# Optimization experiments

Measured on AMD Instinct MI355X. Metric: run time of the kernel, lower is better.

The kernel has to match this reference:

```python
import jax, jax.numpy as jnp
import numpy as np

N_EMBD = 768

def setup_inputs() -> dict:
    key = jax.random.key(0)
    k1, k2, k3, k4 = jax.random.split(key, 4)
    B, T, head_size = 16, 1024, 128
    x = jax.random.normal(k1, (B, T, N_EMBD), dtype=jnp.float32)
    # nn.Linear(in, out, bias=False): weight stored as (out, in); we store transposed (in, out)
    s = 1.0 / np.sqrt(N_EMBD)
    Wk = jax.random.uniform(k2, (N_EMBD, head_size), jnp.float32, -s, s)
    Wq = jax.random.uniform(k3, (N_EMBD, head_size), jnp.float32, -s, s)
    Wv = jax.random.uniform(k4, (N_EMBD, head_size), jnp.float32, -s, s)
    return {"x": x, "Wk": Wk, "Wq": Wq, "Wv": Wv}

def reference(x, Wk, Wq, Wv):
    B, T, C = x.shape  # C == n_embd == 768
    k = jnp.einsum('btc,ch->bth', x, Wk)
    q = jnp.einsum('btc,ch->bth', x, Wq)
    v = jnp.einsum('btc,ch->bth', x, Wv)
    # NOTE: original scales by C**-0.5 with C = n_embd (768), not head_size.
    wei = jnp.einsum('bth,bsh->bts', q, k) * (C ** -0.5)  # (B, T, T)
    causal = jnp.tril(jnp.ones((T, T), dtype=bool))
    wei = jnp.where(causal, wei, -jnp.inf)
    wei = jax.nn.softmax(wei, axis=-1)
    # dropout p=0.0 -> identity
    return jnp.einsum('bts,bsh->bth', wei, v)
```

## Files before the change

kernel.cpp:

```cpp
#include <hip/hip_runtime.h>
#include <hip/hip_bf16.h>
#include <math.h>

#define NTOK   16384
#define NEMBD  768
#define HDIM   128

typedef __attribute__((ext_vector_type(8)))  short short8;
typedef __attribute__((ext_vector_type(16))) float floatx16;

#define MFMA32(a,b,c) __builtin_amdgcn_mfma_f32_32x32x16_bf16(a,b,c,0,0,0)

__device__ __forceinline__ unsigned short f2bf(float f) {
    unsigned u = __float_as_uint(f);
    u += 0x7fff + ((u >> 16) & 1);
    return (unsigned short)(u >> 16);
}
__device__ __forceinline__ unsigned pack2(float a, float b) {
    __hip_bfloat162 h2 = __float22bfloat162_rn(make_float2(a, b));
    union { __hip_bfloat162 h; unsigned u; } c; c.h = h2;
    return c.u;
}
__device__ __forceinline__ unsigned pack2_trunc(float a, float b) {
    return __builtin_amdgcn_perm(__float_as_uint(b), __float_as_uint(a),
                                 0x07060302u);
}
__device__ __forceinline__ void gl_lds16(const void* gptr, void* lptr) {
    __builtin_amdgcn_global_load_lds(
        (const __attribute__((address_space(1))) unsigned int*)gptr,
        (__attribute__((address_space(3))) unsigned int*)lptr, 16, 0, 0);
}

__global__ __launch_bounds__(256) void prep_w(
    const float* __restrict__ Wk, const float* __restrict__ Wq,
    const float* __restrict__ Wv, unsigned short* __restrict__ wt)
{
    __shared__ float T[64 * 65];

    const int tid = threadIdx.x;
    const int bw  = blockIdx.x / 24;
    const int rem = blockIdx.x % 24;
    const int ct  = rem >> 1, dh = rem & 1;
    const int c0  = ct * 64, d0 = dh * 64;
    const float* W = (bw == 0) ? Wk : ((bw == 1) ? Wq : Wv);
    const float scale = (bw == 1)
        ? (0.03608439182435161f * 1.4426950408889634f) : 1.0f;

    #pragma unroll
    for (int pass = 0; pass < 4; ++pass) {
        int idx = pass * 256 + tid;
        int c  = idx >> 4;
        int d4 = idx & 15;
        float4 v = ((const float4*)W)[(size_t)(c0 + c) * 32 + dh * 16 + d4];
        v.x *= scale; v.y *= scale; v.z *= scale; v.w *= scale;
        T[(d4 * 4 + 0) * 65 + c] = v.x;
        T[(d4 * 4 + 1) * 65 + c] = v.y;
        T[(d4 * 4 + 2) * 65 + c] = v.z;
        T[(d4 * 4 + 3) * 65 + c] = v.w;
    }
    __syncthreads();

    #pragma unroll
    for (int pass = 0; pass < 2; ++pass) {
        int idx = pass * 256 + tid;
        int d  = idx >> 3;
        int c8 = idx & 7;
        const float* row = &T[d * 65 + c8 * 8];
        uint4 u = make_uint4(pack2(row[0], row[1]), pack2(row[2], row[3]),
                             pack2(row[4], row[5]), pack2(row[6], row[7]));
        *(uint4*)&wt[(size_t)bw * (HDIM * NEMBD) + (size_t)(d0 + d) * NEMBD
                     + c0 + c8 * 8] = u;
    }
}

__global__ __launch_bounds__(512) void qkv_fused(
    const float* __restrict__ x, const unsigned short* __restrict__ wt,
    unsigned short* __restrict__ kb, unsigned short* __restrict__ qb,
    unsigned short* __restrict__ vT)
{
    __shared__ __align__(16) char As[2][8192];
    __shared__ __align__(16) char Bs[2][16384];

    const int tid = threadIdx.x, w = tid >> 6, lane = tid & 63;
    const int l31 = lane & 31, h = lane >> 5;
    const int r8 = lane >> 3, c8 = lane & 7;
    const int wm = w >> 2, wn = w & 3;
    const int l = blockIdx.x;
    const int low3 = l & 7, rest = l >> 3;
    const int mtile = (rest / 3) * 8 + low3;
    const int nh    = rest % 3;
    const int m0 = mtile * 64;
    const int nbase = nh * 128;
    const int arow = tid >> 3, ac = tid & 7;

    floatx16 acc;
    #pragma unroll
    for (int i = 0; i < 16; ++i) acc[i] = 0.f;

    const float* asrc = x + (size_t)(m0 + arow) * NEMBD + ac * 8;

    #pragma unroll
    for (int j = 0; j < 2; ++j) {
        int rowb = w * 16 + j * 8;
        int row  = rowb + r8;
        gl_lds16((const char*)wt + ((size_t)(nbase + row) * NEMBD) * 2
                     + ((c8 ^ (row & 7)) * 16),
                 Bs[0] + rowb * 128);
    }
    float4 a0 = ((const float4*)asrc)[0];
    float4 a1 = ((const float4*)asrc)[1];
    {
        uint4 u0 = make_uint4(pack2(a0.x, a0.y), pack2(a0.z, a0.w),
                              pack2(a1.x, a1.y), pack2(a1.z, a1.w));
        *(uint4*)(As[0] + arow * 128 + ((ac ^ (arow & 7)) * 16)) = u0;
    }
    {
        const float4* src = (const float4*)(asrc + 64);
        a0 = src[0]; a1 = src[1];
    }
    asm volatile("s_waitcnt lgkmcnt(0)" ::: "memory");
    __builtin_amdgcn_sched_barrier(0);
    __builtin_amdgcn_s_barrier();

    #pragma unroll
    for (int it = 0; it < 12; ++it) {
        char* Acur = As[it & 1];
        char* Bcur = Bs[it & 1];
        char* Anxt = As[(it & 1) ^ 1];
        char* Bnxt = Bs[(it & 1) ^ 1];

        if (it < 11) {
            const int k0n = (it + 1) * 64;
            #pragma unroll
            for (int j = 0; j < 2; ++j) {
                int rowb = w * 16 + j * 8;
                int row  = rowb + r8;
                gl_lds16((const char*)wt
                             + ((size_t)(nbase + row) * NEMBD + k0n) * 2
                             + ((c8 ^ (row & 7)) * 16),
                         Bnxt + rowb * 128);
            }
            uint4 u0 = make_uint4(pack2(a0.x, a0.y), pack2(a0.z, a0.w),
                                  pack2(a1.x, a1.y), pack2(a1.z, a1.w));
            *(uint4*)(Anxt + arow * 128 + ((ac ^ (arow & 7)) * 16)) = u0;
            if (it < 10) {
                const float4* src = (const float4*)(asrc + (it + 2) * 64);
                a0 = src[0]; a1 = src[1];
            }
        }

        const int ar = wm * 32 + l31;
        const int br = wn * 32 + l31;
        #pragma unroll
        for (int ks = 0; ks < 4; ++ks) {
            short8 af = *(const short8*)(Acur + ar * 128
                                         + (((2*ks + h) ^ (ar & 7)) * 16));
            short8 bf = *(const short8*)(Bcur + br * 128
                                         + (((2*ks + h) ^ (br & 7)) * 16));
            acc = MFMA32(af, bf, acc);
        }

        if (it < 10) {
            asm volatile("s_waitcnt vmcnt(2)" ::: "memory");
            asm volatile("s_waitcnt lgkmcnt(0)" ::: "memory");
            __builtin_amdgcn_sched_barrier(0);
            __builtin_amdgcn_s_barrier();
        } else if (it == 10) {
            asm volatile("s_waitcnt vmcnt(0)" ::: "memory");
            asm volatile("s_waitcnt lgkmcnt(0)" ::: "memory");
            __builtin_amdgcn_sched_barrier(0);
            __builtin_amdgcn_s_barrier();
        }
    }

    const int tbase = m0 + wm * 32;
    const int n0loc = wn * 32;
    if (nh < 2) {
        unsigned short* outp = (nh == 0) ? kb : qb;
        int d = n0loc + l31;
        #pragma unroll
        for (int r = 0; r < 16; ++r) {
            int t = tbase + (r & 3) + 8 * (r >> 2) + 4 * h;
            outp[(size_t)t * HDIM + d] = f2bf(acc[r]);
        }
    } else {
        int d = n0loc + l31, b = m0 >> 10, tloc = (m0 & 1023) + wm * 32;
        #pragma unroll
        for (int g = 0; g < 4; ++g) {
            int t = tloc + 8 * g + 4 * h;
            uint2 u = make_uint2(pack2(acc[4*g+0], acc[4*g+1]),
                                 pack2(acc[4*g+2], acc[4*g+3]));
            *(uint2*)((char*)vT + (((size_t)(b * HDIM + d)) * 1024 + t) * 2) = u;
        }
    }
}

__global__ __launch_bounds__(256) void attn_mfma(
    const unsigned short* __restrict__ qb, const unsigned short* __restrict__ kb,
    const unsigned short* __restrict__ vT, float* __restrict__ out)
{
    __shared__ __align__(16) float Obuf[4 * 32 * 128];
    __shared__ float lred[128];

    const int tid = threadIdx.x, w = tid >> 6, lane = tid & 63;
    const int l31 = lane & 31, h = lane >> 5;
    const int u  = blockIdx.x & 255;
    const int b  = u & 15, p = u >> 4;
    const int qt = (blockIdx.x >> 8) ? (31 - p) : p;

    const char* kb_b = (const char*)kb + (size_t)b * (1024 * 256);
    const char* qb_b = (const char*)qb + (size_t)b * (1024 * 256);
    const char* vT_b = (const char*)vT + (size_t)b * (HDIM * 2048);

    short8 qf[8];
    {
        const char* qrow = qb_b + (size_t)(qt * 32 + l31) * 256 + h * 16;
        #pragma unroll
        for (int ks = 0; ks < 8; ++ks)
            qf[ks] = *(const short8*)(qrow + ks * 32);
    }

    floatx16 o[4];
    #pragma unroll
    for (int nt = 0; nt < 4; ++nt)
        #pragma unroll
        for (int i = 0; i < 16; ++i) o[nt][i] = 0.f;
    float l_r = 0.f;

    short8 kf[8];
    if (w <= qt) {
        const char* krow = kb_b + (size_t)(w * 32 + l31) * 256 + h * 16;
        #pragma unroll
        for (int ks = 0; ks < 8; ++ks)
            kf[ks] = *(const short8*)(krow + ks * 32);
    }

    for (int st = w; st <= qt; st += 4) {
        short8 vf[8];
        {
            const char* vrow0 = vT_b + (size_t)l31 * 2048 + (size_t)st * 64 + h * 16;
            #pragma unroll
            for (int nt = 0; nt < 4; ++nt) {
                const char* vr = vrow0 + (size_t)nt * (32 * 2048);
                vf[nt * 2 + 0] = *(const short8*)(vr + 0);
                vf[nt * 2 + 1] = *(const short8*)(vr + 32);
            }
        }
        floatx16 s;
        #pragma unroll
        for (int i = 0; i < 16; ++i) s[i] = 0.f;
        __builtin_amdgcn_s_setprio(1);
        #pragma unroll
        for (int ks = 0; ks < 8; ++ks) s = MFMA32(kf[ks], qf[ks], s);
        __builtin_amdgcn_s_setprio(0);

        if (st + 4 <= qt) {
            const char* krow = kb_b + (size_t)((st + 4) * 32 + l31) * 256 + h * 16;
            #pragma unroll
            for (int ks = 0; ks < 8; ++ks)
                kf[ks] = *(const short8*)(krow + ks * 32);
        }

        if (st == qt) {
            #pragma unroll
            for (int r = 0; r < 16; ++r) {
                int key = (r & 3) + 8 * (r >> 2) + 4 * h;
                if (key > l31) s[r] = -1e30f;
            }
        }
        float p16[16];
        float ps0 = 0.f, ps1 = 0.f, ps2 = 0.f, ps3 = 0.f;
        #pragma unroll
        for (int r = 0; r < 4; ++r) {
            p16[4*r+0] = __builtin_amdgcn_exp2f(s[4*r+0]);
            p16[4*r+1] = __builtin_amdgcn_exp2f(s[4*r+1]);
            p16[4*r+2] = __builtin_amdgcn_exp2f(s[4*r+2]);
            p16[4*r+3] = __builtin_amdgcn_exp2f(s[4*r+3]);
            ps0 += p16[4*r+0]; ps1 += p16[4*r+1];
            ps2 += p16[4*r+2]; ps3 += p16[4*r+3];
        }
        l_r += (ps0 + ps1) + (ps2 + ps3);

        unsigned own[8];
        #pragma unroll
        for (int i = 0; i < 8; ++i) own[i] = pack2_trunc(p16[2*i], p16[2*i+1]);
        asm("v_permlane32_swap_b32 %0, %1" : "+v"(own[0]), "+v"(own[2]));
        asm("v_permlane32_swap_b32 %0, %1" : "+v"(own[1]), "+v"(own[3]));
        asm("v_permlane32_swap_b32 %0, %1" : "+v"(own[4]), "+v"(own[6]));
        asm("v_permlane32_swap_b32 %0, %1" : "+v"(own[5]), "+v"(own[7]));
        short8 pf[2];
        {
            union { short8 v; unsigned uu[4]; } f0, f1;
            f0.uu[0]=own[0]; f0.uu[1]=own[1]; f0.uu[2]=own[2]; f0.uu[3]=own[3];
            f1.uu[0]=own[4]; f1.uu[1]=own[5]; f1.uu[2]=own[6]; f1.uu[3]=own[7];
            pf[0] = f0.v; pf[1] = f1.v;
        }
        __builtin_amdgcn_s_setprio(1);
        #pragma unroll
        for (int nt = 0; nt < 4; ++nt) {
            o[nt] = MFMA32(vf[nt * 2 + 0], pf[0], o[nt]);
            o[nt] = MFMA32(vf[nt * 2 + 1], pf[1], o[nt]);
        }
        __builtin_amdgcn_s_setprio(0);
    }

    l_r += __shfl_xor(l_r, 32, 64);
    if (lane < 32) lred[w * 32 + l31] = l_r;
    {
        float* mybuf = &Obuf[w * 4096];
        #pragma unroll
        for (int nt = 0; nt < 4; ++nt) {
            #pragma unroll
            for (int g = 0; g < 4; ++g) {
                int chunk = nt * 8 + 2 * g + h;
                int slot  = (chunk & 24) | ((chunk & 7) ^ (l31 & 7));
                *((float4*)&mybuf[l31 * 128] + slot) =
                    make_float4(o[nt][4*g+0], o[nt][4*g+1],
                                o[nt][4*g+2], o[nt][4*g+3]);
            }
        }
    }
    __syncthreads();
    {
        int q  = tid >> 3;
        int cb = (tid & 7) * 4;
        float inv = 1.f / (lred[q] + lred[32 + q] + lred[64 + q] + lred[96 + q]);
        #pragma unroll
        for (int cc = 0; cc < 4; ++cc) {
            int chunk = cb + cc;
            int slot  = (chunk & 24) | ((chunk & 7) ^ (q & 7));
            float4 v0 = *((float4*)&Obuf[0 * 4096 + q * 128] + slot);
            float4 v1 = *((float4*)&Obuf[1 * 4096 + q * 128] + slot);
            float4 v2 = *((float4*)&Obuf[2 * 4096 + q * 128] + slot);
            float4 v3 = *((float4*)&Obuf[3 * 4096 + q * 128] + slot);
            float4 v = make_float4((v0.x + v1.x + v2.x + v3.x) * inv,
                                   (v0.y + v1.y + v2.y + v3.y) * inv,
                                   (v0.z + v1.z + v2.z + v3.z) * inv,
                                   (v0.w + v1.w + v2.w + v3.w) * inv);
            *(float4*)&out[((size_t)(b * 1024 + qt * 32 + q)) * HDIM + chunk * 4] = v;
        }
    }
}

extern "C" void kernel_launch(void* const* d_in, const int* in_sizes, int n_in,
                              void* d_out, int out_size, void* d_ws, size_t ws_size,
                              hipStream_t stream)
{
    const float* x  = (const float*)d_in[0];
    const float* Wk = (const float*)d_in[1];
    const float* Wq = (const float*)d_in[2];
    const float* Wv = (const float*)d_in[3];
    float* outp = (float*)d_out;

    char* ws = (char*)d_ws;
    unsigned short* wt = (unsigned short*)(ws);
    unsigned short* kb = (unsigned short*)(ws + 589824);
    unsigned short* qb = (unsigned short*)(ws + 4784128);
    unsigned short* vT = (unsigned short*)(ws + 8978432);

    prep_w<<<72, 256, 0, stream>>>(Wk, Wq, Wv, wt);
    qkv_fused<<<768, 512, 0, stream>>>(x, wt, kb, qb, vT);
    attn_mfma<<<512, 256, 0, stream>>>(qb, kb, vT, outp);
}
```

Measured before the change: 126.1 us.

## Load QKV weight fragments directly into registers via MFMA-ready layout

prep_w now writes the bf16 weights in a per-lane fragment layout that matches the MFMA B-operand order. qkv_fused loads B fragments straight from global memory into double-buffered registers instead of staging them through LDS with global_load_lds. This drops the B shared-memory buffers and their LDS reads, and the vmcnt waits in the loop are removed. The cost is more live registers, and global load latency is now hidden only by the one-iteration register prefetch rather than by explicit waits.

```diff
diff --git a/kernel.cpp b/kernel.cpp
--- a/kernel.cpp
+++ b/kernel.cpp
@@ -24,11 +24,6 @@
 __device__ __forceinline__ unsigned pack2_trunc(float a, float b) {
     return __builtin_amdgcn_perm(__float_as_uint(b), __float_as_uint(a),
                                  0x07060302u);
-}
-__device__ __forceinline__ void gl_lds16(const void* gptr, void* lptr) {
-    __builtin_amdgcn_global_load_lds(
-        (const __attribute__((address_space(1))) unsigned int*)gptr,
-        (__attribute__((address_space(3))) unsigned int*)lptr, 16, 0, 0);
 }
 
 __global__ __launch_bounds__(256) void prep_w(
@@ -41,7 +36,7 @@
     const int bw  = blockIdx.x / 24;
     const int rem = blockIdx.x % 24;
     const int ct  = rem >> 1, dh = rem & 1;
-    const int c0  = ct * 64, d0 = dh * 64;
+    const int c0  = ct * 64;
     const float* W = (bw == 0) ? Wk : ((bw == 1) ? Wq : Wv);
     const float scale = (bw == 1)
         ? (0.03608439182435161f * 1.4426950408889634f) : 1.0f;
@@ -62,14 +57,18 @@
 
     #pragma unroll
     for (int pass = 0; pass < 2; ++pass) {
-        int idx = pass * 256 + tid;
-        int d  = idx >> 3;
-        int c8 = idx & 7;
-        const float* row = &T[d * 65 + c8 * 8];
+        int idx  = pass * 256 + tid;
+        int dloc = idx >> 3;
+        int c8   = idx & 7;
+        const float* row = &T[dloc * 65 + c8 * 8];
         uint4 u = make_uint4(pack2(row[0], row[1]), pack2(row[2], row[3]),
                              pack2(row[4], row[5]), pack2(row[6], row[7]));
-        *(uint4*)&wt[(size_t)bw * (HDIM * NEMBD) + (size_t)(d0 + d) * NEMBD
-                     + c0 + c8 * 8] = u;
+        int kc    = ct * 8 + c8;
+        int ksl   = kc >> 1, hb = kc & 1;
+        int dglob = dh * 64 + dloc;
+        int nt    = dglob >> 5;
+        int lanef = (dglob & 31) + 32 * hb;
+        ((uint4*)wt)[(size_t)((bw * 4 + nt) * 48 + ksl) * 64 + lanef] = u;
     }
 }
 
@@ -79,18 +78,15 @@
     unsigned short* __restrict__ vT)
 {
     __shared__ __align__(16) char As[2][8192];
-    __shared__ __align__(16) char Bs[2][16384];
 
     const int tid = threadIdx.x, w = tid >> 6, lane = tid & 63;
     const int l31 = lane & 31, h = lane >> 5;
-    const int r8 = lane >> 3, c8 = lane & 7;
     const int wm = w >> 2, wn = w & 3;
     const int l = blockIdx.x;
     const int low3 = l & 7, rest = l >> 3;
     const int mtile = (rest / 3) * 8 + low3;
     const int nh    = rest % 3;
     const int m0 = mtile * 64;
-    const int nbase = nh * 128;
     const int arow = tid >> 3, ac = tid & 7;
 
     floatx16 acc;
@@ -98,15 +94,12 @@
     for (int i = 0; i < 16; ++i) acc[i] = 0.f;
 
     const float* asrc = x + (size_t)(m0 + arow) * NEMBD + ac * 8;
-
-    #pragma unroll
-    for (int j = 0; j < 2; ++j) {
-        int rowb = w * 16 + j * 8;
-        int row  = rowb + r8;
-        gl_lds16((const char*)wt + ((size_t)(nbase + row) * NEMBD) * 2
-                     + ((c8 ^ (row & 7)) * 16),
-                 Bs[0] + rowb * 128);
-    }
+    const uint4* wtfb = (const uint4*)wt
+                        + (size_t)(nh * 4 + wn) * 48 * 64 + lane;
+
+    uint4 bq[2][4];
+    #pragma unroll
+    for (int ks = 0; ks < 4; ++ks) bq[0][ks] = wtfb[ks * 64];
     float4 a0 = ((const float4*)asrc)[0];
     float4 a1 = ((const float4*)asrc)[1];
     {
@@ -125,21 +118,12 @@
     #pragma unroll
     for (int it = 0; it < 12; ++it) {
         char* Acur = As[it & 1];
-        char* Bcur = Bs[it & 1];
         char* Anxt = As[(it & 1) ^ 1];
-        char* Bnxt = Bs[(it & 1) ^ 1];
 
         if (it < 11) {
-            const int k0n = (it + 1) * 64;
-            #pragma unroll
-            for (int j = 0; j < 2; ++j) {
-                int rowb = w * 16 + j * 8;
-                int row  = rowb + r8;
-                gl_lds16((const char*)wt
-                             + ((size_t)(nbase + row) * NEMBD + k0n) * 2
-                             + ((c8 ^ (row & 7)) * 16),
-                         Bnxt + rowb * 128);
-            }
+            #pragma unroll
+            for (int ks = 0; ks < 4; ++ks)
+                bq[(it + 1) & 1][ks] = wtfb[((it + 1) * 4 + ks) * 64];
             uint4 u0 = make_uint4(pack2(a0.x, a0.y), pack2(a0.z, a0.w),
                                   pack2(a1.x, a1.y), pack2(a1.z, a1.w));
             *(uint4*)(Anxt + arow * 128 + ((ac ^ (arow & 7)) * 16)) = u0;
@@ -150,23 +134,15 @@
         }
 
         const int ar = wm * 32 + l31;
-        const int br = wn * 32 + l31;
         #pragma unroll
         for (int ks = 0; ks < 4; ++ks) {
             short8 af = *(const short8*)(Acur + ar * 128
-                                         + (((2*ks + h) ^ (ar & 7)) * 16));
-            short8 bf = *(const short8*)(Bcur + br * 128
-                                         + (((2*ks + h) ^ (br & 7)) * 16));
-            acc = MFMA32(af, bf, acc);
-        }
-
-        if (it < 10) {
-            asm volatile("s_waitcnt vmcnt(2)" ::: "memory");
-            asm volatile("s_waitcnt lgkmcnt(0)" ::: "memory");
-            __builtin_amdgcn_sched_barrier(0);
-            __builtin_amdgcn_s_barrier();
-        } else if (it == 10) {
-            asm volatile("s_waitcnt vmcnt(0)" ::: "memory");
+                                         + (((2 * ks + h) ^ (ar & 7)) * 16));
+            union { uint4 q; short8 v; } bb; bb.q = bq[it & 1][ks];
+            acc = MFMA32(af, bb.v, acc);
+        }
+
+        if (it < 11) {
             asm volatile("s_waitcnt lgkmcnt(0)" ::: "memory");
             __builtin_amdgcn_sched_barrier(0);
             __builtin_amdgcn_s_barrier();
```

After: 128.0 us. No clear change (+1.5%).
